# Optimization experiments

Measured on AMD Instinct MI355X. Metric: run time of the kernel, lower is better.

## Reference

```python
import jax, jax.numpy as jnp
import numpy as np

B, S, D, H, E = 8, 4096, 1024, 2048, 8


def setup_inputs() -> dict:
    key = jax.random.key(0)
    ks = jax.random.split(key, 7)
    scale = 0.02
    return {
        "x": jax.random.normal(ks[0], (B, S, D), dtype=jnp.float32),
        "W1": jax.random.normal(ks[1], (E, D, H), dtype=jnp.float32) * scale,
        "b1": jnp.zeros((E, H), dtype=jnp.float32),
        "W2": jax.random.normal(ks[2], (E, H, D), dtype=jnp.float32) * scale,
        "b2": jnp.zeros((E, D), dtype=jnp.float32),
        "Wg": jax.random.normal(ks[3], (D, E), dtype=jnp.float32) * scale,
        "bg": jnp.zeros((E,), dtype=jnp.float32),
    }


def reference(x, W1, b1, W2, b2, Wg, bg):
    # Gating: softmax then top-1 (argmax) routing.
    logits = jnp.einsum("bsd,de->bse", x, Wg) + bg          # [B,S,E]
    probs = jax.nn.softmax(logits, axis=-1)                    # [B,S,E]
    top1 = jnp.argmax(probs, axis=-1)                          # [B,S] int

    out = jnp.zeros_like(x)
    # Fixed, small expert count: loop over experts (jit-friendly, no dynamic
    # shapes). coef zeros out tokens not routed to expert e, matching the
    # masked scatter in the original (unrouted positions stay 0 -> impossible
    # with top-1 over all experts, but semantics are identical).
    for e in range(E):
        coef = jnp.where(top1 == e, probs[..., e], 0.0)[..., None]  # [B,S,1]
        h = jax.nn.gelu(jnp.einsum("bsd,dh->bsh", x, W1[e]) + b1[e],
                        approximate=False)                      # exact GELU, torch default
        y = jnp.einsum("bsh,hd->bsd", h, W2[e]) + b2[e]
        out = out + coef * y
    return out
```

## Files before the change

### kernel.cpp

```cpp
#include <hip/hip_runtime.h>
#include <hip/hip_bf16.h>
#include <math.h>

#define NTOK 32768
#define DD   1024
#define HH   2048
#define EE   8

#define BM 128
#define BN 128
#define BK 64
#define MAXT 264
#define NBLK 128

typedef __bf16 bf16x8 __attribute__((ext_vector_type(8)));
typedef float  f32x4  __attribute__((ext_vector_type(4)));

__device__ __forceinline__ void gload_lds16(const void* g, void* l) {
  __builtin_amdgcn_global_load_lds((__attribute__((address_space(1))) void*)(g),
                                   (__attribute__((address_space(3))) void*)(l),
                                   16, 0, 0);
}

__global__ __launch_bounds__(256) void k_gating(
    const float* __restrict__ x, const float* __restrict__ wg,
    const float* __restrict__ bg, int* __restrict__ eid,
    float* __restrict__ coef)
{
  int lane = threadIdx.x & 63;
  int wave = threadIdx.x >> 6;
  int t0 = blockIdx.x * 8 + wave * 2;

  const float* xr0 = x + (size_t)t0 * DD;
  const float* xr1 = x + (size_t)(t0 + 1) * DD;
  double s0[8] = {}, s1[8] = {};
#pragma unroll
  for (int it = 0; it < 4; ++it) {
    int c0 = it * 256 + lane * 4;
    float4 xa = *(const float4*)(xr0 + c0);
    float4 xb = *(const float4*)(xr1 + c0);
    const float* w = wg + (size_t)c0 * EE;
#pragma unroll
    for (int j = 0; j < 4; ++j) {
      double fa = (double)(&xa.x)[j];
      double fb = (double)(&xb.x)[j];
#pragma unroll
      for (int e2 = 0; e2 < 8; ++e2) {
        double wv = (double)w[j * EE + e2];
        s0[e2] += fa * wv;
        s1[e2] += fb * wv;
      }
    }
  }

  int sel = lane & 1, sel2 = (lane >> 1) & 1, sel3 = (lane >> 2) & 1;
  int e = (lane & 1) * 4 + (lane & 2) + ((lane >> 2) & 1);
  double bge = (double)bg[e];

#pragma unroll
  for (int tk = 0; tk < 2; ++tk) {
    double* s = tk ? s1 : s0;
    double v4[4];
#pragma unroll
    for (int j = 0; j < 4; ++j) {
      double keep = sel ? s[4 + j] : s[j];
      double send = sel ? s[j] : s[4 + j];
      v4[j] = keep + __shfl_xor(send, 1, 64);
    }
    double v2[2];
#pragma unroll
    for (int j = 0; j < 2; ++j) {
      double keep = sel2 ? v4[2 + j] : v4[j];
      double send = sel2 ? v4[j] : v4[2 + j];
      v2[j] = keep + __shfl_xor(send, 2, 64);
    }
    double keep = sel3 ? v2[1] : v2[0];
    double send = sel3 ? v2[0] : v2[1];
    double tt = keep + __shfl_xor(send, 4, 64);
    tt += __shfl_xor(tt, 8, 64);
    tt += __shfl_xor(tt, 16, 64);
    tt += __shfl_xor(tt, 32, 64);
    double logit = tt + bge;
    double ml = logit; int me = e;
#pragma unroll
    for (int d2 = 1; d2 < 8; d2 <<= 1) {
      double ol = __shfl_xor(ml, d2, 64);
      int oe = __shfl_xor(me, d2, 64);
      if (ol > ml || (ol == ml && oe < me)) { ml = ol; me = oe; }
    }
    double se = exp(logit - ml);
#pragma unroll
    for (int d2 = 1; d2 < 8; d2 <<= 1) se += __shfl_xor(se, d2, 64);
    if (lane == 0) {
      eid[t0 + tk] = me;
      coef[t0 + tk] = (float)(1.0 / se);
    }
  }
}

__global__ __launch_bounds__(256) void k_hist(const int* __restrict__ eid,
                                              int* __restrict__ bhist) {
  __shared__ int h[EE];
  if (threadIdx.x < EE) h[threadIdx.x] = 0;
  __syncthreads();
  int t = blockIdx.x * 256 + threadIdx.x;
  atomicAdd(&h[eid[t]], 1);
  __syncthreads();
  if (threadIdx.x < EE) bhist[blockIdx.x * EE + threadIdx.x] = h[threadIdx.x];
}

__global__ void k_scan(const int* __restrict__ bhist, int* __restrict__ offs,
                       int* __restrict__ bbase, int2* __restrict__ tiles) {
  __shared__ int counts_s[EE];
  __shared__ int offs_s[EE + 1];
  int lane = threadIdx.x;
  if (lane < EE) {
    int sum = 0;
    for (int b = 0; b < NBLK; ++b) sum += bhist[b * EE + lane];
    counts_s[lane] = sum;
  }
  __syncthreads();
  if (lane == 0) {
    int a = 0;
    for (int e = 0; e < EE; ++e) { offs_s[e] = a; offs[e] = a; a += counts_s[e]; }
    offs_s[EE] = a; offs[EE] = a;
    int nt = 0;
    for (int e = 0; e < EE; ++e)
      for (int mt = 0; mt * BM < counts_s[e]; ++mt) tiles[nt++] = make_int2(e, mt);
    for (; nt < MAXT; ++nt) tiles[nt] = make_int2(-1, 0);
  }
  __syncthreads();
  if (lane < EE) {
    int run = offs_s[lane];
    for (int b = 0; b < NBLK; ++b) {
      bbase[b * EE + lane] = run;
      run += bhist[b * EE + lane];
    }
  }
}

__global__ __launch_bounds__(256) void k_scatter(const int* __restrict__ eid,
                                                 const int* __restrict__ bbase,
                                                 int* __restrict__ idx) {
  __shared__ int cur[EE];
  if (threadIdx.x < EE) cur[threadIdx.x] = bbase[blockIdx.x * EE + threadIdx.x];
  __syncthreads();
  int t = blockIdx.x * 256 + threadIdx.x;
  int e = eid[t];
  int p = atomicAdd(&cur[e], 1);
  idx[p] = t;
}

__global__ __launch_bounds__(256) void k_xbf(const float* __restrict__ x,
                                             __bf16* __restrict__ xbf) {
  const int n8 = NTOK * DD / 8;
  const int step = gridDim.x * 256;
  for (int i = blockIdx.x * 256 + threadIdx.x; i < n8; i += step) {
    float4 a = *(const float4*)(x + (size_t)i * 8);
    float4 b = *(const float4*)(x + (size_t)i * 8 + 4);
    bf16x8 v;
    v[0] = (__bf16)a.x; v[1] = (__bf16)a.y; v[2] = (__bf16)a.z; v[3] = (__bf16)a.w;
    v[4] = (__bf16)b.x; v[5] = (__bf16)b.y; v[6] = (__bf16)b.z; v[7] = (__bf16)b.w;
    *(bf16x8*)(xbf + (size_t)i * 8) = v;
  }
}

__global__ __launch_bounds__(256) void k_transpose(
    const float* __restrict__ w, __bf16* __restrict__ wt, int R, int C)
{
  __shared__ float tile[32][33];
  int e = blockIdx.z;
  int c0 = blockIdx.x * 32, rb = blockIdx.y * 256;
  const float* we = w + (size_t)e * R * C;
  __bf16* wte = wt + (size_t)e * R * C;
  int tx = threadIdx.x & 31, ty = threadIdx.x >> 5;
  for (int s = 0; s < 8; ++s) {
    int r0 = rb + s * 32;
#pragma unroll
    for (int j = 0; j < 32; j += 8)
      tile[ty + j][tx] = we[(size_t)(r0 + ty + j) * C + (c0 + tx)];
    __syncthreads();
#pragma unroll
    for (int j = 0; j < 32; j += 8)
      wte[(size_t)(c0 + ty + j) * R + (r0 + tx)] = (__bf16)tile[tx][ty + j];
    __syncthreads();
  }
}

__global__ __launch_bounds__(256) void k_gemm1(
    const __bf16* __restrict__ xbf, const __bf16* __restrict__ w1t,
    const float* __restrict__ b1, const int* __restrict__ idx,
    const int* __restrict__ offs, const int2* __restrict__ tiles,
    __bf16* __restrict__ hbuf)
{
  int2 te = tiles[blockIdx.x];
  int e = te.x;
  if (e < 0) return;
  int mt = te.y, nt = blockIdx.y;
  int off = offs[e], cnt = offs[e + 1] - off;
  int n0 = nt * BN;

  __shared__ __align__(16) unsigned short sA[BM * BK];
  __shared__ __align__(16) unsigned short sB[BN * BK];
  char* sAc = (char*)sA;
  char* sBc = (char*)sB;

  const int tid = threadIdx.x;
  const int lane = tid & 63;
  const int wid = tid >> 6;
  const int wrow = (wid >> 1) * 64, wcol = (wid & 1) * 64;
  const int lr = lane & 15, lk = lane >> 4;

  int tokr[4];
#pragma unroll
  for (int i = 0; i < 4; ++i) {
    int row = (i * 256 + tid) >> 3;
    int rl = mt * BM + row; if (rl >= cnt) rl = cnt - 1;
    tokr[i] = idx[off + rl];
  }

  const char* bsrc = (const char*)(w1t + ((size_t)e * HH + n0) * DD);

  f32x4 acc[4][4] = {};

  for (int k0 = 0; k0 < DD; k0 += BK) {
#pragma unroll
    for (int i = 0; i < 4; ++i) {
      int q = i * 256 + tid;
      int row = q >> 3;
      int ch = (q & 7) ^ (row & 7);
      gload_lds16((const char*)xbf + ((size_t)tokr[i] * DD + k0) * 2 + ch * 16,
                  sAc + q * 16);
    }
#pragma unroll
    for (int i = 0; i < 4; ++i) {
      int q = i * 256 + tid;
      int row = q >> 3;
      int ch = (q & 7) ^ (row & 7);
      gload_lds16(bsrc + (size_t)row * (DD * 2) + (size_t)k0 * 2 + ch * 16,
                  sBc + q * 16);
    }
    __syncthreads();

    bf16x8 af[2][4], bfr[2][4];
#pragma unroll
    for (int kk = 0; kk < 2; ++kk) {
#pragma unroll
      for (int m = 0; m < 4; ++m) {
        int row = wrow + m * 16 + lr;
        af[kk][m] = *(const bf16x8*)(sAc + row * 128 + (((kk * 4 + lk) ^ (row & 7)) * 16));
      }
#pragma unroll
      for (int n = 0; n < 4; ++n) {
        int row = wcol + n * 16 + lr;
        bfr[kk][n] = *(const bf16x8*)(sBc + row * 128 + (((kk * 4 + lk) ^ (row & 7)) * 16));
      }
    }
#pragma unroll
    for (int kk = 0; kk < 2; ++kk)
#pragma unroll
      for (int m = 0; m < 4; ++m)
#pragma unroll
        for (int n = 0; n < 4; ++n)
          acc[m][n] = __builtin_amdgcn_mfma_f32_16x16x32_bf16(af[kk][m], bfr[kk][n], acc[m][n], 0, 0, 0);
    __syncthreads();
  }

#pragma unroll
  for (int m = 0; m < 4; ++m) {
    int rbase = mt * BM + wrow + m * 16 + lk * 4;
#pragma unroll
    for (int n = 0; n < 4; ++n) {
      int col = n0 + wcol + n * 16 + lr;
      float bias = b1[e * HH + col];
#pragma unroll
      for (int j2 = 0; j2 < 4; ++j2) {
        int r2 = rbase + j2;
        if (r2 < cnt) {
          float vv = acc[m][n][j2] + bias;
          float g = 0.5f * vv * (1.0f + erff(vv * 0.70710678118654752f));
          hbuf[(size_t)(off + r2) * HH + col] = (__bf16)g;
        }
      }
    }
  }
}

__global__ __launch_bounds__(256) void k_gemm2(
    const __bf16* __restrict__ hbuf, const __bf16* __restrict__ w2t,
    const float* __restrict__ b2, const int* __restrict__ idx,
    const int* __restrict__ offs, const int2* __restrict__ tiles,
    const float* __restrict__ coef, float* __restrict__ out)
{
  int2 te = tiles[blockIdx.x];
  int e = te.x;
  if (e < 0) return;
  int mt = te.y, nt = blockIdx.y;
  int off = offs[e], cnt = offs[e + 1] - off;
  int n0 = nt * BN;

  __shared__ __align__(16) unsigned short sA[BM * BK];
  __shared__ __align__(16) unsigned short sB[BN * BK];
  char* sAc = (char*)sA;
  char* sBc = (char*)sB;

  const int tid = threadIdx.x;
  const int lane = tid & 63;
  const int wid = tid >> 6;
  const int wrow = (wid >> 1) * 64, wcol = (wid & 1) * 64;
  const int lr = lane & 15, lk = lane >> 4;

  int arow[4];
#pragma unroll
  for (int i = 0; i < 4; ++i) {
    int row = (i * 256 + tid) >> 3;
    int rl = mt * BM + row; if (rl >= cnt) rl = cnt - 1;
    arow[i] = off + rl;
  }

  const char* bsrc = (const char*)(w2t + ((size_t)e * DD + n0) * HH);

  f32x4 acc[4][4] = {};

  for (int k0 = 0; k0 < HH; k0 += BK) {
#pragma unroll
    for (int i = 0; i < 4; ++i) {
      int q = i * 256 + tid;
      int ch = (q & 7) ^ ((q >> 3) & 7);
      gload_lds16((const char*)hbuf + ((size_t)arow[i] * HH + k0) * 2 + ch * 16,
                  sAc + q * 16);
    }
#pragma unroll
    for (int i = 0; i < 4; ++i) {
      int q = i * 256 + tid;
      int row = q >> 3;
      int ch = (q & 7) ^ (row & 7);
      gload_lds16(bsrc + (size_t)row * (HH * 2) + (size_t)k0 * 2 + ch * 16,
                  sBc + q * 16);
    }
    __syncthreads();

    bf16x8 af[2][4], bfr[2][4];
#pragma unroll
    for (int kk = 0; kk < 2; ++kk) {
#pragma unroll
      for (int m = 0; m < 4; ++m) {
        int row = wrow + m * 16 + lr;
        af[kk][m] = *(const bf16x8*)(sAc + row * 128 + (((kk * 4 + lk) ^ (row & 7)) * 16));
      }
#pragma unroll
      for (int n = 0; n < 4; ++n) {
        int row = wcol + n * 16 + lr;
        bfr[kk][n] = *(const bf16x8*)(sBc + row * 128 + (((kk * 4 + lk) ^ (row & 7)) * 16));
      }
    }
#pragma unroll
    for (int kk = 0; kk < 2; ++kk)
#pragma unroll
      for (int m = 0; m < 4; ++m)
#pragma unroll
        for (int n = 0; n < 4; ++n)
          acc[m][n] = __builtin_amdgcn_mfma_f32_16x16x32_bf16(af[kk][m], bfr[kk][n], acc[m][n], 0, 0, 0);
    __syncthreads();
  }

#pragma unroll
  for (int m = 0; m < 4; ++m) {
    int rbase = mt * BM + wrow + m * 16 + lk * 4;
#pragma unroll
    for (int j2 = 0; j2 < 4; ++j2) {
      int r2 = rbase + j2;
      if (r2 < cnt) {
        int t = idx[off + r2];
        float cf = coef[t];
#pragma unroll
        for (int n = 0; n < 4; ++n) {
          int col = n0 + wcol + n * 16 + lr;
          out[(size_t)t * DD + col] = cf * (acc[m][n][j2] + b2[e * DD + col]);
        }
      }
    }
  }
}

extern "C" void kernel_launch(void* const* d_in, const int* in_sizes, int n_in,
                              void* d_out, int out_size, void* d_ws, size_t ws_size,
                              hipStream_t stream)
{
  const float* x  = (const float*)d_in[0];
  const float* W1 = (const float*)d_in[1];
  const float* b1 = (const float*)d_in[2];
  const float* W2 = (const float*)d_in[3];
  const float* b2 = (const float*)d_in[4];
  const float* Wg = (const float*)d_in[5];
  const float* bg = (const float*)d_in[6];
  float* out = (float*)d_out;

  char* ws = (char*)d_ws;
  size_t o = 0;
  int* offs   = (int*)(ws + o); o += 64;
  int2* tiles = (int2*)(ws + o); o += MAXT * 8;
  int* bhist  = (int*)(ws + o); o += NBLK * EE * 4;
  int* bbase  = (int*)(ws + o); o += NBLK * EE * 4;
  int* eid    = (int*)(ws + o); o += (size_t)NTOK * 4;
  float* coef = (float*)(ws + o); o += (size_t)NTOK * 4;
  int* idx    = (int*)(ws + o); o += (size_t)NTOK * 4;
  o = (o + 255) & ~(size_t)255;
  __bf16* xbf = (__bf16*)(ws + o); o += (size_t)NTOK * DD * 2;
  __bf16* w1t = (__bf16*)(ws + o); o += (size_t)EE * HH * DD * 2;
  __bf16* w2t = (__bf16*)(ws + o); o += (size_t)EE * DD * HH * 2;
  __bf16* hbuf = (__bf16*)(ws + o); o += (size_t)NTOK * HH * 2;

  k_gating<<<NTOK / 8, 256, 0, stream>>>(x, Wg, bg, eid, coef);
  k_hist<<<NBLK, 256, 0, stream>>>(eid, bhist);
  k_scan<<<1, 64, 0, stream>>>(bhist, offs, bbase, tiles);
  k_scatter<<<NBLK, 256, 0, stream>>>(eid, bbase, idx);
  k_xbf<<<2048, 256, 0, stream>>>(x, xbf);
  k_transpose<<<dim3(HH / 32, DD / 256, EE), 256, 0, stream>>>(W1, w1t, DD, HH);
  k_transpose<<<dim3(DD / 32, HH / 256, EE), 256, 0, stream>>>(W2, w2t, HH, DD);
  k_gemm1<<<dim3(MAXT, HH / BN), 256, 0, stream>>>(xbf, w1t, b1, idx, offs, tiles, hbuf);
  k_gemm2<<<dim3(MAXT, DD / BN), 256, 0, stream>>>(hbuf, w2t, b2, idx, offs, tiles, coef, out);
}
```

Measured before the change: 883.7 us.

## Use 256x256 double-buffered GEMM tiles with 512 threads and fuse bf16 cast into gating

Both expert GEMMs move from 128x128 single-buffered tiles with 4 waves to 256x256 tiles with 8 waves and a double-buffered LDS pipeline, prefetching the next K slice while computing the current one. MFMA sections get raised wave priority. The separate x-to-bf16 conversion kernel is removed and the cast is done inside the gating kernel, which already reads x. The larger tiles raise arithmetic intensity and cut redundant loads, at the cost of 128KB of LDS per block, higher register pressure, and more padding waste on each expert's partial last tile.

New measurement: 876.6 us. No clear change (-0.8%).

```diff
diff --git a/kernel.cpp b/kernel.cpp
--- a/kernel.cpp
+++ b/kernel.cpp
@@ -7,13 +7,14 @@
 #define HH   2048
 #define EE   8
 
-#define BM 128
-#define BN 128
+#define BM 256
+#define BN 256
 #define BK 64
-#define MAXT 264
+#define MAXT2 144
 #define NBLK 128
 
 typedef __bf16 bf16x8 __attribute__((ext_vector_type(8)));
+typedef __bf16 bf16x4 __attribute__((ext_vector_type(4)));
 typedef float  f32x4  __attribute__((ext_vector_type(4)));
 
 __device__ __forceinline__ void gload_lds16(const void* g, void* l) {
@@ -25,7 +26,7 @@
 __global__ __launch_bounds__(256) void k_gating(
     const float* __restrict__ x, const float* __restrict__ wg,
     const float* __restrict__ bg, int* __restrict__ eid,
-    float* __restrict__ coef)
+    float* __restrict__ coef, __bf16* __restrict__ xbf)
 {
   int lane = threadIdx.x & 63;
   int wave = threadIdx.x >> 6;
@@ -39,6 +40,11 @@
     int c0 = it * 256 + lane * 4;
     float4 xa = *(const float4*)(xr0 + c0);
     float4 xb = *(const float4*)(xr1 + c0);
+    bf16x4 ca, cb;
+#pragma unroll
+    for (int j = 0; j < 4; ++j) { ca[j] = (__bf16)(&xa.x)[j]; cb[j] = (__bf16)(&xb.x)[j]; }
+    *(bf16x4*)(xbf + (size_t)t0 * DD + c0) = ca;
+    *(bf16x4*)(xbf + (size_t)(t0 + 1) * DD + c0) = cb;
     const float* w = wg + (size_t)c0 * EE;
 #pragma unroll
     for (int j = 0; j < 4; ++j) {
@@ -127,7 +133,7 @@
     int nt = 0;
     for (int e = 0; e < EE; ++e)
       for (int mt = 0; mt * BM < counts_s[e]; ++mt) tiles[nt++] = make_int2(e, mt);
-    for (; nt < MAXT; ++nt) tiles[nt] = make_int2(-1, 0);
+    for (; nt < MAXT2; ++nt) tiles[nt] = make_int2(-1, 0);
   }
   __syncthreads();
   if (lane < EE) {
@@ -149,20 +155,6 @@
   int e = eid[t];
   int p = atomicAdd(&cur[e], 1);
   idx[p] = t;
-}
-
-__global__ __launch_bounds__(256) void k_xbf(const float* __restrict__ x,
-                                             __bf16* __restrict__ xbf) {
-  const int n8 = NTOK * DD / 8;
-  const int step = gridDim.x * 256;
-  for (int i = blockIdx.x * 256 + threadIdx.x; i < n8; i += step) {
-    float4 a = *(const float4*)(x + (size_t)i * 8);
-    float4 b = *(const float4*)(x + (size_t)i * 8 + 4);
-    bf16x8 v;
-    v[0] = (__bf16)a.x; v[1] = (__bf16)a.y; v[2] = (__bf16)a.z; v[3] = (__bf16)a.w;
-    v[4] = (__bf16)b.x; v[5] = (__bf16)b.y; v[6] = (__bf16)b.z; v[7] = (__bf16)b.w;
-    *(bf16x8*)(xbf + (size_t)i * 8) = v;
-  }
 }
 
 __global__ __launch_bounds__(256) void k_transpose(
@@ -187,7 +179,7 @@
   }
 }
 
-__global__ __launch_bounds__(256) void k_gemm1(
+__global__ __launch_bounds__(512, 2) void k_gemm1(
     const __bf16* __restrict__ xbf, const __bf16* __restrict__ w1t,
     const float* __restrict__ b1, const int* __restrict__ idx,
     const int* __restrict__ offs, const int2* __restrict__ tiles,
@@ -200,93 +192,104 @@
   int off = offs[e], cnt = offs[e + 1] - off;
   int n0 = nt * BN;
 
-  __shared__ __align__(16) unsigned short sA[BM * BK];
-  __shared__ __align__(16) unsigned short sB[BN * BK];
-  char* sAc = (char*)sA;
-  char* sBc = (char*)sB;
+  __shared__ __align__(16) char smem[131072];
+  char* sA = smem;
+  char* sB = smem + 65536;
 
   const int tid = threadIdx.x;
   const int lane = tid & 63;
   const int wid = tid >> 6;
-  const int wrow = (wid >> 1) * 64, wcol = (wid & 1) * 64;
+  const int wr = wid >> 2, wc = wid & 3;
   const int lr = lane & 15, lk = lane >> 4;
 
-  int tokr[4];
+  int tokr[4], srow[4], sch[4];
 #pragma unroll
   for (int i = 0; i < 4; ++i) {
-    int row = (i * 256 + tid) >> 3;
+    int q = i * 512 + tid;
+    int row = q >> 3;
+    srow[i] = row;
+    sch[i] = (q & 7) ^ (row & 7);
     int rl = mt * BM + row; if (rl >= cnt) rl = cnt - 1;
     tokr[i] = idx[off + rl];
   }
-
   const char* bsrc = (const char*)(w1t + ((size_t)e * HH + n0) * DD);
 
-  f32x4 acc[4][4] = {};
-
-  for (int k0 = 0; k0 < DD; k0 += BK) {
-#pragma unroll
-    for (int i = 0; i < 4; ++i) {
-      int q = i * 256 + tid;
-      int row = q >> 3;
-      int ch = (q & 7) ^ (row & 7);
-      gload_lds16((const char*)xbf + ((size_t)tokr[i] * DD + k0) * 2 + ch * 16,
-                  sAc + q * 16);
-    }
-#pragma unroll
-    for (int i = 0; i < 4; ++i) {
-      int q = i * 256 + tid;
-      int row = q >> 3;
-      int ch = (q & 7) ^ (row & 7);
-      gload_lds16(bsrc + (size_t)row * (DD * 2) + (size_t)k0 * 2 + ch * 16,
-                  sBc + q * 16);
+  f32x4 acc[8][4] = {};
+
+#pragma unroll
+  for (int i = 0; i < 4; ++i)
+    gload_lds16((const char*)xbf + ((size_t)tokr[i] * DD) * 2 + sch[i] * 16,
+                sA + (i * 512 + tid) * 16);
+#pragma unroll
+  for (int i = 0; i < 4; ++i)
+    gload_lds16(bsrc + (size_t)srow[i] * (DD * 2) + sch[i] * 16,
+                sB + (i * 512 + tid) * 16);
+  __syncthreads();
+
+  int cur = 0;
+  for (int kt = 0; kt < DD / BK; ++kt) {
+    if (kt + 1 < DD / BK) {
+      int k0 = (kt + 1) * BK;
+      char* dA = sA + (cur ^ 1) * 32768;
+      char* dB = sB + (cur ^ 1) * 32768;
+#pragma unroll
+      for (int i = 0; i < 4; ++i)
+        gload_lds16((const char*)xbf + ((size_t)tokr[i] * DD + k0) * 2 + sch[i] * 16,
+                    dA + (i * 512 + tid) * 16);
+#pragma unroll
+      for (int i = 0; i < 4; ++i)
+        gload_lds16(bsrc + (size_t)srow[i] * (DD * 2) + (size_t)k0 * 2 + sch[i] * 16,
+                    dB + (i * 512 + tid) * 16);
+    }
+    __builtin_amdgcn_sched_barrier(0);
+    const char* cAb = sA + cur * 32768;
+    const char* cBb = sB + cur * 32768;
+#pragma unroll
+    for (int kk = 0; kk < 2; ++kk) {
+      bf16x8 af[8], bf[4];
+#pragma unroll
+      for (int m = 0; m < 8; ++m) {
+        int row = wr * 128 + m * 16 + lr;
+        af[m] = *(const bf16x8*)(cAb + row * 128 + (((kk * 4 + lk) ^ (row & 7)) * 16));
+      }
+#pragma unroll
+      for (int n = 0; n < 4; ++n) {
+        int row = wc * 64 + n * 16 + lr;
+        bf[n] = *(const bf16x8*)(cBb + row * 128 + (((kk * 4 + lk) ^ (row & 7)) * 16));
+      }
+      __builtin_amdgcn_s_setprio(1);
+#pragma unroll
+      for (int m = 0; m < 8; ++m)
+#pragma unroll
+        for (int n = 0; n < 4; ++n)
+          acc[m][n] = __builtin_amdgcn_mfma_f32_16x16x32_bf16(af[m], bf[n], acc[m][n], 0, 0, 0);
+      __builtin_amdgcn_s_setprio(0);
     }
     __syncthreads();
-
-    bf16x8 af[2][4], bfr[2][4];
-#pragma unroll
-    for (int kk = 0; kk < 2; ++kk) {
-#pragma unroll
-      for (int m = 0; m < 4; ++m) {
-        int row = wrow + m * 16 + lr;
-        af[kk][m] = *(const bf16x8*)(sAc + row * 128 + (((kk * 4 + lk) ^ (row & 7)) * 16));
-      }
-#pragma unroll
-      for (int n = 0; n < 4; ++n) {
-        int row = wcol + n * 16 + lr;
-        bfr[kk][n] = *(const bf16x8*)(sBc + row * 128 + (((kk * 4 + lk) ^ (row & 7)) * 16));
-      }
-    }
-#pragma unroll
-    for (int kk = 0; kk < 2; ++kk)
-#pragma unroll
-      for (int m = 0; m < 4; ++m)
-#pragma unroll
-        for (int n = 0; n < 4; ++n)
-          acc[m][n] = __builtin_amdgcn_mfma_f32_16x16x32_bf16(af[kk][m], bfr[kk][n], acc[m][n], 0, 0, 0);
-    __syncthreads();
-  }
-
-#pragma unroll
-  for (int m = 0; m < 4; ++m) {
-    int rbase = mt * BM + wrow + m * 16 + lk * 4;
+    cur ^= 1;
+  }
+
+#pragma unroll
+  for (int m = 0; m < 8; ++m) {
+    int rb = mt * BM + wr * 128 + m * 16 + lk * 4;
 #pragma unroll
     for (int n = 0; n < 4; ++n) {
-      int col = n0 + wcol + n * 16 + lr;
+      int col = n0 + wc * 64 + n * 16 + lr;
       float bias = b1[e * HH + col];
 #pragma unroll
-      for (int j2 = 0; j2 < 4; ++j2) {
-        int r2 = rbase + j2;
-        if (r2 < cnt) {
-          float vv = acc[m][n][j2] + bias;
+      for (int j = 0; j < 4; ++j) {
+        int r = rb + j;
+        if (r < cnt) {
+          float vv = acc[m][n][j] + bias;
           float g = 0.5f * vv * (1.0f + erff(vv * 0.70710678118654752f));
-          hbuf[(size_t)(off + r2) * HH + col] = (__bf16)g;
+          hbuf[(size_t)(off + r) * HH + col] = (__bf16)g;
         }
       }
     }
   }
 }
 
-__global__ __launch_bounds__(256) void k_gemm2(
+__global__ __launch_bounds__(512, 2) void k_gemm2(
     const __bf16* __restrict__ hbuf, const __bf16* __restrict__ w2t,
     const float* __restrict__ b2, const int* __restrict__ idx,
     const int* __restrict__ offs, const int2* __restrict__ tiles,
@@ -299,84 +302,96 @@
   int off = offs[e], cnt = offs[e + 1] - off;
   int n0 = nt * BN;
 
-  __shared__ __align__(16) unsigned short sA[BM * BK];
-  __shared__ __align__(16) unsigned short sB[BN * BK];
-  char* sAc = (char*)sA;
-  char* sBc = (char*)sB;
+  __shared__ __align__(16) char smem[131072];
+  char* sA = smem;
+  char* sB = smem + 65536;
 
   const int tid = threadIdx.x;
   const int lane = tid & 63;
   const int wid = tid >> 6;
-  const int wrow = (wid >> 1) * 64, wcol = (wid & 1) * 64;
+  const int wr = wid >> 2, wc = wid & 3;
   const int lr = lane & 15, lk = lane >> 4;
 
-  int arow[4];
+  int arow[4], srow[4], sch[4];
 #pragma unroll
   for (int i = 0; i < 4; ++i) {
-    int row = (i * 256 + tid) >> 3;
+    int q = i * 512 + tid;
+    int row = q >> 3;
+    srow[i] = row;
+    sch[i] = (q & 7) ^ (row & 7);
     int rl = mt * BM + row; if (rl >= cnt) rl = cnt - 1;
     arow[i] = off + rl;
   }
-
   const char* bsrc = (const char*)(w2t + ((size_t)e * DD + n0) * HH);
 
-  f32x4 acc[4][4] = {};
-
-  for (int k0 = 0; k0 < HH; k0 += BK) {
-#pragma unroll
-    for (int i = 0; i < 4; ++i) {
-      int q = i * 256 + tid;
-      int ch = (q & 7) ^ ((q >> 3) & 7);
-      gload_lds16((const char*)hbuf + ((size_t)arow[i] * HH + k0) * 2 + ch * 16,
-                  sAc + q * 16);
-    }
-#pragma unroll
-    for (int i = 0; i < 4; ++i) {
-      int q = i * 256 + tid;
-      int row = q >> 3;
-      int ch = (q & 7) ^ (row & 7);
-      gload_lds16(bsrc + (size_t)row * (HH * 2) + (size_t)k0 * 2 + ch * 16,
-                  sBc + q * 16);
+  f32x4 acc[8][4] = {};
+
+#pragma unroll
+  for (int i = 0; i < 4; ++i)
+    gload_lds16((const char*)hbuf + ((size_t)arow[i] * HH) * 2 + sch[i] * 16,
+                sA + (i * 512 + tid) * 16);
+#pragma unroll
+  for (int i = 0; i < 4; ++i)
+    gload_lds16(bsrc + (size_t)srow[i] * (HH * 2) + sch[i] * 16,
+                sB + (i * 512 + tid) * 16);
+  __syncthreads();
+
+  int cur = 0;
+  for (int kt = 0; kt < HH / BK; ++kt) {
+    if (kt + 1 < HH / BK) {
+      int k0 = (kt + 1) * BK;
+      char* dA = sA + (cur ^ 1) * 32768;
+      char* dB = sB + (cur ^ 1) * 32768;
+#pragma unroll
+      for (int i = 0; i < 4; ++i)
+        gload_lds16((const char*)hbuf + ((size_t)arow[i] * HH + k0) * 2 + sch[i] * 16,
+                    dA + (i * 512 + tid) * 16);
+#pragma unroll
+      for (int i = 0; i < 4; ++i)
+        gload_lds16(bsrc + (size_t)srow[i] * (HH * 2) + (size_t)k0 * 2 + sch[i] * 16,
+                    dB + (i * 512 + tid) * 16);
+    }
+    __builtin_amdgcn_sched_barrier(0);
+    const char* cAb = sA + cur * 32768;
+    const char* cBb = sB + cur * 32768;
+#pragma unroll
+    for (int kk = 0; kk < 2; ++kk) {
+      bf16x8 af[8], bf[4];
+#pragma unroll
+      for (int m = 0; m < 8; ++m) {
+        int row = wr * 128 + m * 16 + lr;
+        af[m] = *(const bf16x8*)(cAb + row * 128 + (((kk * 4 + lk) ^ (row & 7)) * 16));
+      }
+#pragma unroll
+      for (int n = 0; n < 4; ++n) {
+        int row = wc * 64 + n * 16 + lr;
+        bf[n] = *(const bf16x8*)(cBb + row * 128 + (((kk * 4 + lk) ^ (row & 7)) * 16));
+      }
+      __builtin_amdgcn_s_setprio(1);
+#pragma unroll
+      for (int m = 0; m < 8; ++m)
+#pragma unroll
+        for (int n = 0; n < 4; ++n)
+          acc[m][n] = __builtin_amdgcn_mfma_f32_16x16x32_bf16(af[m], bf[n], acc[m][n], 0, 0, 0);
+      __builtin_amdgcn_s_setprio(0);
     }
     __syncthreads();
-
-    bf16x8 af[2][4], bfr[2][4];
-#pragma unroll
-    for (int kk = 0; kk < 2; ++kk) {
-#pragma unroll
-      for (int m = 0; m < 4; ++m) {
-        int row = wrow + m * 16 + lr;
-        af[kk][m] = *(const bf16x8*)(sAc + row * 128 + (((kk * 4 + lk) ^ (row & 7)) * 16));
-      }
-#pragma unroll
-      for (int n = 0; n < 4; ++n) {
-        int row = wcol + n * 16 + lr;
-        bfr[kk][n] = *(const bf16x8*)(sBc + row * 128 + (((kk * 4 + lk) ^ (row & 7)) * 16));
-      }
-    }
-#pragma unroll
-    for (int kk = 0; kk < 2; ++kk)
-#pragma unroll
-      for (int m = 0; m < 4; ++m)
-#pragma unroll
-        for (int n = 0; n < 4; ++n)
-          acc[m][n] = __builtin_amdgcn_mfma_f32_16x16x32_bf16(af[kk][m], bfr[kk][n], acc[m][n], 0, 0, 0);
-    __syncthreads();
-  }
-
-#pragma unroll
-  for (int m = 0; m < 4; ++m) {
-    int rbase = mt * BM + wrow + m * 16 + lk * 4;
-#pragma unroll
-    for (int j2 = 0; j2 < 4; ++j2) {
-      int r2 = rbase + j2;
-      if (r2 < cnt) {
-        int t = idx[off + r2];
+    cur ^= 1;
+  }
+
+#pragma unroll
+  for (int m = 0; m < 8; ++m) {
+    int rb = mt * BM + wr * 128 + m * 16 + lk * 4;
+#pragma unroll
+    for (int j = 0; j < 4; ++j) {
+      int r = rb + j;
+      if (r < cnt) {
+        int t = idx[off + r];
         float cf = coef[t];
 #pragma unroll
         for (int n = 0; n < 4; ++n) {
-          int col = n0 + wcol + n * 16 + lr;
-          out[(size_t)t * DD + col] = cf * (acc[m][n][j2] + b2[e * DD + col]);
+          int col = n0 + wc * 64 + n * 16 + lr;
+          out[(size_t)t * DD + col] = cf * (acc[m][n][j] + b2[e * DD + col]);
         }
       }
     }
@@ -399,7 +414,7 @@
   char* ws = (char*)d_ws;
   size_t o = 0;
   int* offs   = (int*)(ws + o); o += 64;
-  int2* tiles = (int2*)(ws + o); o += MAXT * 8;
+  int2* tiles = (int2*)(ws + o); o += MAXT2 * 8;
   int* bhist  = (int*)(ws + o); o += NBLK * EE * 4;
   int* bbase  = (int*)(ws + o); o += NBLK * EE * 4;
   int* eid    = (int*)(ws + o); o += (size_t)NTOK * 4;
@@ -411,13 +426,12 @@
   __bf16* w2t = (__bf16*)(ws + o); o += (size_t)EE * DD * HH * 2;
   __bf16* hbuf = (__bf16*)(ws + o); o += (size_t)NTOK * HH * 2;
 
-  k_gating<<<NTOK / 8, 256, 0, stream>>>(x, Wg, bg, eid, coef);
+  k_gating<<<NTOK / 8, 256, 0, stream>>>(x, Wg, bg, eid, coef, xbf);
   k_hist<<<NBLK, 256, 0, stream>>>(eid, bhist);
   k_scan<<<1, 64, 0, stream>>>(bhist, offs, bbase, tiles);
   k_scatter<<<NBLK, 256, 0, stream>>>(eid, bbase, idx);
-  k_xbf<<<2048, 256, 0, stream>>>(x, xbf);
   k_transpose<<<dim3(HH / 32, DD / 256, EE), 256, 0, stream>>>(W1, w1t, DD, HH);
   k_transpose<<<dim3(DD / 32, HH / 256, EE), 256, 0, stream>>>(W2, w2t, HH, DD);
-  k_gemm1<<<dim3(MAXT, HH / BN), 256, 0, stream>>>(xbf, w1t, b1, idx, offs, tiles, hbuf);
-  k_gemm2<<<dim3(MAXT, DD / BN), 256, 0, stream>>>(hbuf, w2t, b2, idx, offs, tiles, coef, out);
-}
+  k_gemm1<<<dim3(MAXT2, HH / BN), 512, 0, stream>>>(xbf, w1t, b1, idx, offs, tiles, hbuf);
+  k_gemm2<<<dim3(MAXT2, DD / BN), 512, 0, stream>>>(hbuf, w2t, b2, idx, offs, tiles, coef, out);
+}
```
